# Optimization experiments

Hardware: AMD Instinct MI355X
Metric: run time of the kernel (lower is better)

## Reference

```python
import jax, jax.numpy as jnp
import numpy as np


def setup_inputs() -> dict:
    key = jax.random.key(0)
    k1, k2, k3 = jax.random.split(key, 3)
    B, S, E = 4, 4096, 512
    x = jax.random.normal(k1, (B, S, E), dtype=jnp.float32)
    # xavier_uniform for Linear weights; zero biases (per _reset_parameters)
    lim_qkv = float(np.sqrt(6.0 / (E + 3 * E)))
    W_qkv = jax.random.uniform(k2, (3 * E, E), minval=-lim_qkv, maxval=lim_qkv, dtype=jnp.float32)
    b_qkv = jnp.zeros((3 * E,), dtype=jnp.float32)
    lim_out = float(np.sqrt(6.0 / (E + E)))
    W_out = jax.random.uniform(k3, (E, E), minval=-lim_out, maxval=lim_out, dtype=jnp.float32)
    b_out = jnp.zeros((E,), dtype=jnp.float32)
    return {"x": x, "W_qkv": W_qkv, "b_qkv": b_qkv, "W_out": W_out, "b_out": b_out}


def reference(x, W_qkv, b_qkv, W_out, b_out):
    B, S, E = x.shape
    H = 8
    D = E // H
    qkv = x @ W_qkv.T + b_qkv                      # [B,S,3E]
    qkv = qkv.reshape(B, S, H, 3 * D)
    q, k, v = jnp.split(qkv, 3, axis=-1)            # each [B,S,H,D]
    q = jax.nn.sigmoid(q)
    k = jax.nn.sigmoid(k)
    # flow conservation normalizers (sum over seq dim=1, then feature dim=3)
    i = jnp.sum(q * jnp.sum(k, axis=1, keepdims=True), axis=3, keepdims=True)      # [B,S,H,1]
    o = jnp.sum(k * jnp.sum(q, axis=1, keepdims=True), axis=3, keepdims=True)
    i_hat = jnp.sum(q * jnp.sum(k / o, axis=1, keepdims=True), axis=3, keepdims=True)
    o_hat = jnp.sum(k * jnp.sum(q / i, axis=1, keepdims=True), axis=3, keepdims=True)
    # NOTE: faithful to source — matmul batches over (B,S) and contracts the HEAD axis
    vw = v * jax.nn.softmax(o_hat, axis=1)          # [B,S,H,D]
    kv = jnp.einsum('bshd,bshe->bsde', k, vw)       # [B,S,D,D]
    r = jnp.einsum('bshd,bsde->bshe', q / i, kv) * jax.nn.sigmoid(i_hat)  # [B,S,H,D]
    values = r.reshape(B, S, E)
    return values @ W_out.T + b_out
```

## Files before the change

### kernel.cpp

```cpp
#include <hip/hip_runtime.h>
#include <cstdint>
#include <cstddef>

#define B_ 4
#define S_ 4096
#define E_ 512
#define NPOS 16384
#define QKVC 1536
#define K_ 512

typedef unsigned short u16;
typedef u16    u16x8  __attribute__((ext_vector_type(8)));
typedef u16    u16x4  __attribute__((ext_vector_type(4)));
typedef __bf16 bf16x8 __attribute__((ext_vector_type(8)));
typedef float  f32x4  __attribute__((ext_vector_type(4)));

__device__ __forceinline__ u16 f2bf(float f) {
    unsigned u = __builtin_bit_cast(unsigned, f);
    unsigned r = (u + 0x7fffu + ((u >> 16) & 1u)) >> 16;
    return (u16)r;
}
__device__ __forceinline__ float bf2f(u16 u) {
    return __builtin_bit_cast(float, (unsigned)u << 16);
}
__device__ __forceinline__ float rcpf(float x) { return __builtin_amdgcn_rcpf(x); }

__device__ __forceinline__ void async16(const void* g, void* lds) {
    __builtin_amdgcn_global_load_lds(
        (const __attribute__((address_space(1))) unsigned int*)g,
        (__attribute__((address_space(3))) unsigned int*)lds, 16, 0, 0);
}

__global__ void cvt_kernel(const float4* __restrict__ in, u16x4* __restrict__ out, int n4) {
    int i = blockIdx.x * 256 + threadIdx.x;
    if (i < n4) {
        float4 v = in[i];
        u16x4 o;
        o[0] = f2bf(v.x); o[1] = f2bf(v.y); o[2] = f2bf(v.z); o[3] = f2bf(v.w);
        out[i] = o;
    }
}

__device__ __forceinline__ void mfma_step(const u16* AsB, const u16* BsB,
                                          int wm, int wn, int fr, int fkk,
                                          f32x4 (&acc)[4][4]) {
    bf16x8 a[4], b[4];
    #pragma unroll
    for (int i = 0; i < 4; ++i)
        a[i] = *(const bf16x8*)&AsB[(wm + i * 16 + fr) * 32 + fkk];
    #pragma unroll
    for (int j = 0; j < 4; ++j)
        b[j] = *(const bf16x8*)&BsB[(wn + j * 16 + fr) * 32 + fkk];
    __builtin_amdgcn_s_setprio(1);
    #pragma unroll
    for (int i = 0; i < 4; ++i)
        #pragma unroll
        for (int j = 0; j < 4; ++j)
            acc[i][j] = __builtin_amdgcn_mfma_f32_16x16x32_bf16(a[i], b[j], acc[i][j], 0, 0, 0);
    __builtin_amdgcn_s_setprio(0);
}

__global__ __launch_bounds__(256) void gemm_qkv(
        const u16* __restrict__ A, const u16* __restrict__ Bw,
        const float* __restrict__ bias,
        u16* __restrict__ Qb, u16* __restrict__ Kb, u16* __restrict__ Vb,
        int K) {
    __shared__ u16 As[2][128 * 32];
    __shared__ u16 Bs[2][128 * 32];
    const int tid  = threadIdx.x;
    const int wave = tid >> 6, lane = tid & 63;
    const int m0 = blockIdx.y * 128, n0 = blockIdx.x * 128;
    const int wm = (wave & 1) * 64, wn = (wave >> 1) * 64;

    const int srow = wave * 16 + (lane >> 2);
    const int cgs  = (lane & 3) ^ ((lane >> 2) & 3) ^ ((lane >> 4) & 3);
    const u16* Ap = A  + (size_t)(m0 + srow) * K + cgs * 8;
    const u16* Bp = Bw + (size_t)(n0 + srow) * K + cgs * 8;
    const int woff = wave * 512;
    const size_t rstep = (size_t)64 * K;

    f32x4 acc[4][4] = {};
    const int fr  = lane & 15;
    const int fkk = (((lane >> 4) ^ (fr & 3) ^ ((fr >> 2) & 3))) * 8;

    async16(Ap,         &As[0][woff]);
    async16(Ap + rstep, &As[0][woff + 2048]);
    async16(Bp,         &Bs[0][woff]);
    async16(Bp + rstep, &Bs[0][woff + 2048]);
    __syncthreads();

    int cur = 0;
    for (int k0 = 32; k0 < K; k0 += 32) {
        const int nxt = cur ^ 1;
        async16(Ap + k0,         &As[nxt][woff]);
        async16(Ap + k0 + rstep, &As[nxt][woff + 2048]);
        async16(Bp + k0,         &Bs[nxt][woff]);
        async16(Bp + k0 + rstep, &Bs[nxt][woff + 2048]);
        mfma_step(As[cur], Bs[cur], wm, wn, fr, fkk, acc);
        __syncthreads();
        cur = nxt;
    }
    mfma_step(As[cur], Bs[cur], wm, wn, fr, fkk, acc);

    const int cn = lane & 15, rb = (lane >> 4) * 4;
    const int cg   = (n0 + wn) >> 6;
    const int type = cg % 3;
    const int hb   = cg / 3;
    u16* dst = (type == 0) ? Qb : (type == 1) ? Kb : Vb;
    const bool sg = (type < 2);
    #pragma unroll
    for (int i = 0; i < 4; ++i) {
        int mbase = m0 + wm + i * 16 + rb;
        #pragma unroll
        for (int j = 0; j < 4; ++j) {
            int ccol = j * 16 + cn;
            float bv = bias[n0 + wn + ccol];
            int outcol = hb * 64 + ccol;
            f32x4 av = acc[i][j];
            #pragma unroll
            for (int r = 0; r < 4; ++r) {
                float v = av[r] + bv;
                if (sg) v = 1.f / (1.f + __expf(-v));
                dst[(size_t)(mbase + r) * 512 + outcol] = f2bf(v);
            }
        }
    }
}

__global__ __launch_bounds__(256) void gemm_out(
        const u16* __restrict__ A, const u16* __restrict__ Bw,
        const float* __restrict__ bias, float* __restrict__ C,
        int N, int K) {
    __shared__ u16 As[2][128 * 32];
    __shared__ u16 Bs[2][128 * 32];
    const int tid  = threadIdx.x;
    const int wave = tid >> 6, lane = tid & 63;
    const int m0 = blockIdx.y * 128, n0 = blockIdx.x * 128;
    const int wm = (wave & 1) * 64, wn = (wave >> 1) * 64;
    const int srow = wave * 16 + (lane >> 2);
    const int cgs  = (lane & 3) ^ ((lane >> 2) & 3) ^ ((lane >> 4) & 3);
    const u16* Ap = A  + (size_t)(m0 + srow) * K + cgs * 8;
    const u16* Bp = Bw + (size_t)(n0 + srow) * K + cgs * 8;
    const int woff = wave * 512;
    const size_t rstep = (size_t)64 * K;
    f32x4 acc[4][4] = {};
    const int fr  = lane & 15;
    const int fkk = (((lane >> 4) ^ (fr & 3) ^ ((fr >> 2) & 3))) * 8;

    async16(Ap,         &As[0][woff]);
    async16(Ap + rstep, &As[0][woff + 2048]);
    async16(Bp,         &Bs[0][woff]);
    async16(Bp + rstep, &Bs[0][woff + 2048]);
    __syncthreads();

    int cur = 0;
    for (int k0 = 32; k0 < K; k0 += 32) {
        const int nxt = cur ^ 1;
        async16(Ap + k0,         &As[nxt][woff]);
        async16(Ap + k0 + rstep, &As[nxt][woff + 2048]);
        async16(Bp + k0,         &Bs[nxt][woff]);
        async16(Bp + k0 + rstep, &Bs[nxt][woff + 2048]);
        mfma_step(As[cur], Bs[cur], wm, wn, fr, fkk, acc);
        __syncthreads();
        cur = nxt;
    }
    mfma_step(As[cur], Bs[cur], wm, wn, fr, fkk, acc);

    const int cn = lane & 15, rb = (lane >> 4) * 4;
    #pragma unroll
    for (int i = 0; i < 4; ++i) {
        int mbase = m0 + wm + i * 16 + rb;
        #pragma unroll
        for (int j = 0; j < 4; ++j) {
            int nn = n0 + wn + j * 16 + cn;
            float bv = bias[nn];
            f32x4 av = acc[i][j];
            #pragma unroll
            for (int r = 0; r < 4; ++r)
                C[(size_t)(mbase + r) * N + nn] = av[r] + bv;
        }
    }
}

__global__ __launch_bounds__(256) void sum_qk(const u16* __restrict__ Qg, const u16* __restrict__ Kg,
                                              float* __restrict__ sumq, float* __restrict__ sumk) {
    int b = blockIdx.x, sc = blockIdx.y;
    int w = threadIdx.x >> 6, lane = threadIdx.x & 63;
    float aq[8] = {}, ak[8] = {};
    int p0 = b * S_ + sc * 32 + w * 8;
    for (int it = 0; it < 8; ++it) {
        size_t off = (size_t)(p0 + it) * 512 + lane * 8;
        u16x8 q8 = *(const u16x8*)(Qg + off);
        u16x8 k8 = *(const u16x8*)(Kg + off);
        #pragma unroll
        for (int j = 0; j < 8; ++j) { aq[j] += bf2f(q8[j]); ak[j] += bf2f(k8[j]); }
    }
    __shared__ float red[4][1024];
    #pragma unroll
    for (int j = 0; j < 8; ++j) {
        red[w][lane * 8 + j]       = aq[j];
        red[w][512 + lane * 8 + j] = ak[j];
    }
    __syncthreads();
    int t = threadIdx.x;
    #pragma unroll
    for (int rr = 0; rr < 4; ++rr) {
        int slot = rr * 256 + t;
        float s = red[0][slot] + red[1][slot] + red[2][slot] + red[3][slot];
        float* dst = (slot < 512) ? &sumq[b * 512 + slot] : &sumk[b * 512 + (slot - 512)];
        atomicAdd(dst, s);
    }
}

__global__ __launch_bounds__(256) void fused_io(const u16* __restrict__ Qg, const u16* __restrict__ Kg,
                                                const float* __restrict__ sumq, const float* __restrict__ sumk,
                                                float* __restrict__ iv,
                                                float* __restrict__ sumqi, float* __restrict__ sumko) {
    int b = blockIdx.x, sc = blockIdx.y;
    int w = threadIdx.x >> 6, lane = threadIdx.x & 63;
    float skL[8], sqL[8];
    #pragma unroll
    for (int j = 0; j < 8; ++j) {
        skL[j] = sumk[b * 512 + lane * 8 + j];
        sqL[j] = sumq[b * 512 + lane * 8 + j];
    }
    float aqi[8] = {}, ako[8] = {};
    int p0 = b * S_ + sc * 32 + w * 8;
    for (int it = 0; it < 8; ++it) {
        int p = p0 + it;
        size_t off = (size_t)p * 512 + lane * 8;
        u16x8 q8 = *(const u16x8*)(Qg + off);
        u16x8 k8 = *(const u16x8*)(Kg + off);
        float qf[8], kf[8];
        #pragma unroll
        for (int j = 0; j < 8; ++j) { qf[j] = bf2f(q8[j]); kf[j] = bf2f(k8[j]); }
        float di = 0.f, dox = 0.f;
        #pragma unroll
        for (int j = 0; j < 8; ++j) { di += qf[j] * skL[j]; dox += kf[j] * sqL[j]; }
        di  += __shfl_xor(di, 1);  di  += __shfl_xor(di, 2);  di  += __shfl_xor(di, 4);
        dox += __shfl_xor(dox, 1); dox += __shfl_xor(dox, 2); dox += __shfl_xor(dox, 4);
        if ((lane & 7) == 0) iv[(size_t)p * 8 + (lane >> 3)] = di;
        float ri = rcpf(di), ro = rcpf(dox);
        #pragma unroll
        for (int j = 0; j < 8; ++j) { aqi[j] += qf[j] * ri; ako[j] += kf[j] * ro; }
    }
    __shared__ float red[4][1024];
    #pragma unroll
    for (int j = 0; j < 8; ++j) {
        red[w][lane * 8 + j]       = aqi[j];
        red[w][512 + lane * 8 + j] = ako[j];
    }
    __syncthreads();
    int t = threadIdx.x;
    #pragma unroll
    for (int rr = 0; rr < 4; ++rr) {
        int slot = rr * 256 + t;
        float s = red[0][slot] + red[1][slot] + red[2][slot] + red[3][slot];
        float* dst = (slot < 512) ? &sumqi[b * 512 + slot] : &sumko[b * 512 + (slot - 512)];
        atomicAdd(dst, s);
    }
}

__global__ __launch_bounds__(256) void io2_kernel(const u16* __restrict__ Qg, const u16* __restrict__ Kg,
                                                  const float* __restrict__ sumqi, const float* __restrict__ sumko,
                                                  const float* __restrict__ iv,
                                                  float* __restrict__ rowsc, float* __restrict__ wexp,
                                                  float* __restrict__ sm) {
    int b = blockIdx.x, sc = blockIdx.y;
    int w = threadIdx.x >> 6, lane = threadIdx.x & 63;
    float skoL[8], sqiL[8];
    #pragma unroll
    for (int j = 0; j < 8; ++j) {
        skoL[j] = sumko[b * 512 + lane * 8 + j];
        sqiL[j] = sumqi[b * 512 + lane * 8 + j];
    }
    float smacc = 0.f;
    int p0 = b * S_ + sc * 32 + w * 8;
    for (int it = 0; it < 8; ++it) {
        int p = p0 + it;
        size_t off = (size_t)p * 512 + lane * 8;
        u16x8 q8 = *(const u16x8*)(Qg + off);
        u16x8 k8 = *(const u16x8*)(Kg + off);
        float dih = 0.f, doh = 0.f;
        #pragma unroll
        for (int j = 0; j < 8; ++j) {
            dih += bf2f(q8[j]) * skoL[j];
            doh += bf2f(k8[j]) * sqiL[j];
        }
        dih += __shfl_xor(dih, 1); dih += __shfl_xor(dih, 2); dih += __shfl_xor(dih, 4);
        doh += __shfl_xor(doh, 1); doh += __shfl_xor(doh, 2); doh += __shfl_xor(doh, 4);
        if ((lane & 7) == 0) {
            int h = lane >> 3;
            float sig = 1.f / (1.f + __expf(-dih));
            rowsc[(size_t)p * 8 + h] = sig * rcpf(iv[(size_t)p * 8 + h]);
            float we = __expf(fminf(doh, 80.f));
            wexp[(size_t)p * 8 + h] = we;
            smacc += we;
        }
    }
    __shared__ float sr[4][8];
    if ((lane & 7) == 0) sr[w][lane >> 3] = smacc;
    __syncthreads();
    if (threadIdx.x < 8)
        atomicAdd(&sm[b * 8 + threadIdx.x],
                  sr[0][threadIdx.x] + sr[1][threadIdx.x] + sr[2][threadIdx.x] + sr[3][threadIdx.x]);
}

__global__ __launch_bounds__(256) void finalize_kernel(
        const u16* __restrict__ Qg, const u16* __restrict__ Kg, const u16* __restrict__ Vg,
        const float* __restrict__ rowsc, const float* __restrict__ wexp, const float* __restrict__ sm,
        u16* __restrict__ Rg) {
    __shared__ float Ml[4][2][8][9];
    __shared__ float vw[4][2][8][68];
    int w = threadIdx.x >> 6, lane = threadIdx.x & 63;
    int p0 = (blockIdx.x * 4 + w) * 2;
    int b = p0 >> 12;

    {
        int pl = (lane >> 3) & 1, hh = lane & 7, quad = lane >> 4;
        const u16* qa = Qg + (size_t)(p0 + pl) * 512 + hh * 64 + quad * 8;
        const u16* ka = Kg + (size_t)(p0 + pl) * 512 + hh * 64 + quad * 8;
        bf16x8 a0 = __builtin_bit_cast(bf16x8, *(const u16x8*)qa);
        bf16x8 a1 = __builtin_bit_cast(bf16x8, *(const u16x8*)(qa + 32));
        bf16x8 b0 = __builtin_bit_cast(bf16x8, *(const u16x8*)ka);
        bf16x8 b1 = __builtin_bit_cast(bf16x8, *(const u16x8*)(ka + 32));
        f32x4 accm = {0.f, 0.f, 0.f, 0.f};
        accm = __builtin_amdgcn_mfma_f32_16x16x32_bf16(a0, b0, accm, 0, 0, 0);
        accm = __builtin_amdgcn_mfma_f32_16x16x32_bf16(a1, b1, accm, 0, 0, 0);
        if (((lane >> 5) & 1) == ((lane >> 3) & 1)) {
            int plm = lane >> 5, hr = ((lane >> 4) & 1) * 4, h2 = lane & 7;
            #pragma unroll
            for (int r = 0; r < 4; ++r) Ml[w][plm][hr + r][h2] = accm[r];
        }
    }
    {
        int hv = lane >> 3, e0 = (lane & 7) * 8;
        float invsm = rcpf(sm[b * 8 + hv]);
        #pragma unroll
        for (int pl = 0; pl < 2; ++pl) {
            u16x8 v8 = *(const u16x8*)(Vg + (size_t)(p0 + pl) * 512 + lane * 8);
            float wgt = wexp[(size_t)(p0 + pl) * 8 + hv] * invsm;
            f32x4 x0, x1;
            #pragma unroll
            for (int j = 0; j < 4; ++j) { x0[j] = bf2f(v8[j]) * wgt; x1[j] = bf2f(v8[4 + j]) * wgt; }
            *(f32x4*)&vw[w][pl][hv][e0]     = x0;
            *(f32x4*)&vw[w][pl][hv][e0 + 4] = x1;
        }
    }
    __syncthreads();
    {
        int pl = lane >> 5, idx = lane & 31, h = idx >> 2, eq = (idx & 3) * 16;
        float out[16] = {};
        #pragma unroll
        for (int h2 = 0; h2 < 8; ++h2) {
            float m = Ml[w][pl][h][h2];
            #pragma unroll
            for (int c = 0; c < 4; ++c) {
                f32x4 vv = *(const f32x4*)&vw[w][pl][h2][eq + c * 4];
                #pragma unroll
                for (int j = 0; j < 4; ++j) out[c * 4 + j] += m * vv[j];
            }
        }
        float rs = rowsc[(size_t)(p0 + pl) * 8 + h];
        u16x8 o0, o1;
        #pragma unroll
        for (int j = 0; j < 8; ++j) { o0[j] = f2bf(out[j] * rs); o1[j] = f2bf(out[8 + j] * rs); }
        u16* dst = Rg + (size_t)(p0 + pl) * 512 + h * 64 + eq;
        *(u16x8*)dst       = o0;
        *(u16x8*)(dst + 8) = o1;
    }
}

extern "C" void kernel_launch(void* const* d_in, const int* in_sizes, int n_in,
                              void* d_out, int out_size, void* d_ws, size_t ws_size,
                              hipStream_t stream) {
    const float* x    = (const float*)d_in[0];
    const float* Wqkv = (const float*)d_in[1];
    const float* bqkv = (const float*)d_in[2];
    const float* Wout = (const float*)d_in[3];
    const float* bout = (const float*)d_in[4];
    float* out = (float*)d_out;
    char* ws = (char*)d_ws;

    constexpr size_t SZ_XBF  = (size_t)NPOS * E_ * 2;
    constexpr size_t SZ_WQBF = (size_t)QKVC * E_ * 2;
    constexpr size_t SZ_WOBF = (size_t)E_ * E_ * 2;
    constexpr size_t SZ_QKVB = (size_t)NPOS * E_ * 2;
    constexpr size_t SZ_SUM  = (size_t)B_ * 512 * 4;
    constexpr size_t SZ_V8   = (size_t)NPOS * 8 * 4;

    size_t off = 0;
    u16*   xbf   = (u16*)(ws + off);   off += SZ_XBF;
    u16*   wqbf  = (u16*)(ws + off);   off += SZ_WQBF;
    u16*   wobf  = (u16*)(ws + off);   off += SZ_WOBF;
    u16*   Qb    = (u16*)(ws + off);   off += SZ_QKVB;
    u16*   Kb    = (u16*)(ws + off);   off += SZ_QKVB;
    u16*   Vb    = (u16*)(ws + off);   off += SZ_QKVB;
    char*  zbase = ws + off;
    float* sumq  = (float*)(ws + off); off += SZ_SUM;
    float* sumk  = (float*)(ws + off); off += SZ_SUM;
    float* sumqi = (float*)(ws + off); off += SZ_SUM;
    float* sumko = (float*)(ws + off); off += SZ_SUM;
    float* sm    = (float*)(ws + off); off += 256;
    size_t zlen  = (char*)(ws + off) - zbase;
    float* iv    = (float*)(ws + off); off += SZ_V8;
    float* rowsc = (float*)(ws + off); off += SZ_V8;
    float* wexp  = (float*)(ws + off); off += SZ_V8;
    u16*   rbf   = xbf;

    hipMemsetAsync(zbase, 0, zlen, stream);

    cvt_kernel<<<(NPOS * E_ / 4) / 256, 256, 0, stream>>>((const float4*)x, (u16x4*)xbf, NPOS * E_ / 4);
    cvt_kernel<<<(QKVC * E_ / 4) / 256, 256, 0, stream>>>((const float4*)Wqkv, (u16x4*)wqbf, QKVC * E_ / 4);
    cvt_kernel<<<(E_ * E_ / 4) / 256, 256, 0, stream>>>((const float4*)Wout, (u16x4*)wobf, E_ * E_ / 4);

    gemm_qkv<<<dim3(QKVC / 128, NPOS / 128), 256, 0, stream>>>(xbf, wqbf, bqkv, Qb, Kb, Vb, K_);

    sum_qk<<<dim3(B_, 128), 256, 0, stream>>>(Qb, Kb, sumq, sumk);
    fused_io<<<dim3(B_, 128), 256, 0, stream>>>(Qb, Kb, sumq, sumk, iv, sumqi, sumko);
    io2_kernel<<<dim3(B_, 128), 256, 0, stream>>>(Qb, Kb, sumqi, sumko, iv, rowsc, wexp, sm);
    finalize_kernel<<<NPOS / 8, 256, 0, stream>>>(Qb, Kb, Vb, rowsc, wexp, sm, rbf);

    gemm_out<<<dim3(E_ / 128, NPOS / 128), 256, 0, stream>>>(rbf, wobf, bout, out, E_, K_);
}
```

Before: 200.8 us.

## Triple-buffer GEMM pipeline and fuse seq-sum of sigmoid Q/K into QKV epilogue

Replaces the double-buffered K loop in both GEMMs with a three-stage async-load pipeline that waits with partial vmcnt and a raw barrier, so global loads for tile t+2 overlap compute on tile t. It also accumulates per-column sums of the sigmoid Q and K values in the QKV GEMM epilogue and reduces them with atomics, which removes the separate sum_qk kernel and its re-read of Q and K. The cost is more LDS per block, which may lower occupancy, plus extra atomics. The sums are taken from fp32 values before bf16 rounding, so they differ slightly from the old sums.

```diff
diff --git a/kernel.cpp b/kernel.cpp
--- a/kernel.cpp
+++ b/kernel.cpp
@@ -60,13 +60,39 @@
     __builtin_amdgcn_s_setprio(0);
 }
 
+#define GEMM_PIPELINE(NT)                                                     \
+    {                                                                          \
+        STAGE(0, 0);                                                           \
+        STAGE(1, 1);                                                           \
+        asm volatile("s_waitcnt vmcnt(4)" ::: "memory");                       \
+        __builtin_amdgcn_s_barrier();                                          \
+        __builtin_amdgcn_sched_barrier(0);                                     \
+        int cb = 0, sb = 1;                                                    \
+        for (int t = 0; t < (NT) - 2; ++t) {                                   \
+            sb = (sb == 2) ? 0 : sb + 1;                                       \
+            STAGE(t + 2, sb);                                                  \
+            mfma_step(As[cb], Bs[cb], wm, wn, fr, fkk, acc);                   \
+            asm volatile("s_waitcnt vmcnt(4)" ::: "memory");                   \
+            __builtin_amdgcn_s_barrier();                                      \
+            __builtin_amdgcn_sched_barrier(0);                                 \
+            cb = (cb == 2) ? 0 : cb + 1;                                       \
+        }                                                                      \
+        mfma_step(As[cb], Bs[cb], wm, wn, fr, fkk, acc);                       \
+        asm volatile("s_waitcnt vmcnt(0)" ::: "memory");                       \
+        __builtin_amdgcn_s_barrier();                                          \
+        __builtin_amdgcn_sched_barrier(0);                                     \
+        cb = (cb == 2) ? 0 : cb + 1;                                           \
+        mfma_step(As[cb], Bs[cb], wm, wn, fr, fkk, acc);                       \
+    }
+
 __global__ __launch_bounds__(256) void gemm_qkv(
         const u16* __restrict__ A, const u16* __restrict__ Bw,
         const float* __restrict__ bias,
         u16* __restrict__ Qb, u16* __restrict__ Kb, u16* __restrict__ Vb,
+        float* __restrict__ sumq, float* __restrict__ sumk,
         int K) {
-    __shared__ u16 As[2][128 * 32];
-    __shared__ u16 Bs[2][128 * 32];
+    __shared__ u16 As[3][128 * 32];
+    __shared__ u16 Bs[3][128 * 32];
     const int tid  = threadIdx.x;
     const int wave = tid >> 6, lane = tid & 63;
     const int m0 = blockIdx.y * 128, n0 = blockIdx.x * 128;
@@ -83,24 +109,15 @@
     const int fr  = lane & 15;
     const int fkk = (((lane >> 4) ^ (fr & 3) ^ ((fr >> 2) & 3))) * 8;
 
-    async16(Ap,         &As[0][woff]);
-    async16(Ap + rstep, &As[0][woff + 2048]);
-    async16(Bp,         &Bs[0][woff]);
-    async16(Bp + rstep, &Bs[0][woff + 2048]);
-    __syncthreads();
-
-    int cur = 0;
-    for (int k0 = 32; k0 < K; k0 += 32) {
-        const int nxt = cur ^ 1;
-        async16(Ap + k0,         &As[nxt][woff]);
-        async16(Ap + k0 + rstep, &As[nxt][woff + 2048]);
-        async16(Bp + k0,         &Bs[nxt][woff]);
-        async16(Bp + k0 + rstep, &Bs[nxt][woff + 2048]);
-        mfma_step(As[cur], Bs[cur], wm, wn, fr, fkk, acc);
-        __syncthreads();
-        cur = nxt;
-    }
-    mfma_step(As[cur], Bs[cur], wm, wn, fr, fkk, acc);
+    #define STAGE(t, buf)                                             \
+        async16(Ap + (t) * 32,         &As[buf][woff]);               \
+        async16(Ap + (t) * 32 + rstep, &As[buf][woff + 2048]);        \
+        async16(Bp + (t) * 32,         &Bs[buf][woff]);               \
+        async16(Bp + (t) * 32 + rstep, &Bs[buf][woff + 2048]);
+
+    const int nt = K >> 5;
+    GEMM_PIPELINE(nt)
+    #undef STAGE
 
     const int cn = lane & 15, rb = (lane >> 4) * 4;
     const int cg   = (n0 + wn) >> 6;
@@ -108,6 +125,7 @@
     const int hb   = cg / 3;
     u16* dst = (type == 0) ? Qb : (type == 1) ? Kb : Vb;
     const bool sg = (type < 2);
+    float colsum[4] = {};
     #pragma unroll
     for (int i = 0; i < 4; ++i) {
         int mbase = m0 + wm + i * 16 + rb;
@@ -120,9 +138,21 @@
             #pragma unroll
             for (int r = 0; r < 4; ++r) {
                 float v = av[r] + bv;
-                if (sg) v = 1.f / (1.f + __expf(-v));
+                if (sg) { v = 1.f / (1.f + __expf(-v)); colsum[j] += v; }
                 dst[(size_t)(mbase + r) * 512 + outcol] = f2bf(v);
             }
+        }
+    }
+    if (sg) {
+        float* sdst = (type == 0) ? sumq : sumk;
+        const int b = m0 >> 12;
+        #pragma unroll
+        for (int j = 0; j < 4; ++j) {
+            float s = colsum[j];
+            s += __shfl_xor(s, 16);
+            s += __shfl_xor(s, 32);
+            if (lane < 16)
+                atomicAdd(&sdst[b * 512 + hb * 64 + j * 16 + cn], s);
         }
     }
 }
@@ -131,8 +161,8 @@
         const u16* __restrict__ A, const u16* __restrict__ Bw,
         const float* __restrict__ bias, float* __restrict__ C,
         int N, int K) {
-    __shared__ u16 As[2][128 * 32];
-    __shared__ u16 Bs[2][128 * 32];
+    __shared__ u16 As[3][128 * 32];
+    __shared__ u16 Bs[3][128 * 32];
     const int tid  = threadIdx.x;
     const int wave = tid >> 6, lane = tid & 63;
     const int m0 = blockIdx.y * 128, n0 = blockIdx.x * 128;
@@ -147,24 +177,15 @@
     const int fr  = lane & 15;
     const int fkk = (((lane >> 4) ^ (fr & 3) ^ ((fr >> 2) & 3))) * 8;
 
-    async16(Ap,         &As[0][woff]);
-    async16(Ap + rstep, &As[0][woff + 2048]);
-    async16(Bp,         &Bs[0][woff]);
-    async16(Bp + rstep, &Bs[0][woff + 2048]);
-    __syncthreads();
-
-    int cur = 0;
-    for (int k0 = 32; k0 < K; k0 += 32) {
-        const int nxt = cur ^ 1;
-        async16(Ap + k0,         &As[nxt][woff]);
-        async16(Ap + k0 + rstep, &As[nxt][woff + 2048]);
-        async16(Bp + k0,         &Bs[nxt][woff]);
-        async16(Bp + k0 + rstep, &Bs[nxt][woff + 2048]);
-        mfma_step(As[cur], Bs[cur], wm, wn, fr, fkk, acc);
-        __syncthreads();
-        cur = nxt;
-    }
-    mfma_step(As[cur], Bs[cur], wm, wn, fr, fkk, acc);
+    #define STAGE(t, buf)                                             \
+        async16(Ap + (t) * 32,         &As[buf][woff]);               \
+        async16(Ap + (t) * 32 + rstep, &As[buf][woff + 2048]);        \
+        async16(Bp + (t) * 32,         &Bs[buf][woff]);               \
+        async16(Bp + (t) * 32 + rstep, &Bs[buf][woff + 2048]);
+
+    const int nt = K >> 5;
+    GEMM_PIPELINE(nt)
+    #undef STAGE
 
     const int cn = lane & 15, rb = (lane >> 4) * 4;
     #pragma unroll
@@ -179,36 +200,6 @@
             for (int r = 0; r < 4; ++r)
                 C[(size_t)(mbase + r) * N + nn] = av[r] + bv;
         }
-    }
-}
-
-__global__ __launch_bounds__(256) void sum_qk(const u16* __restrict__ Qg, const u16* __restrict__ Kg,
-                                              float* __restrict__ sumq, float* __restrict__ sumk) {
-    int b = blockIdx.x, sc = blockIdx.y;
-    int w = threadIdx.x >> 6, lane = threadIdx.x & 63;
-    float aq[8] = {}, ak[8] = {};
-    int p0 = b * S_ + sc * 32 + w * 8;
-    for (int it = 0; it < 8; ++it) {
-        size_t off = (size_t)(p0 + it) * 512 + lane * 8;
-        u16x8 q8 = *(const u16x8*)(Qg + off);
-        u16x8 k8 = *(const u16x8*)(Kg + off);
-        #pragma unroll
-        for (int j = 0; j < 8; ++j) { aq[j] += bf2f(q8[j]); ak[j] += bf2f(k8[j]); }
-    }
-    __shared__ float red[4][1024];
-    #pragma unroll
-    for (int j = 0; j < 8; ++j) {
-        red[w][lane * 8 + j]       = aq[j];
-        red[w][512 + lane * 8 + j] = ak[j];
-    }
-    __syncthreads();
-    int t = threadIdx.x;
-    #pragma unroll
-    for (int rr = 0; rr < 4; ++rr) {
-        int slot = rr * 256 + t;
-        float s = red[0][slot] + red[1][slot] + red[2][slot] + red[3][slot];
-        float* dst = (slot < 512) ? &sumq[b * 512 + slot] : &sumk[b * 512 + (slot - 512)];
-        atomicAdd(dst, s);
     }
 }
 
@@ -414,9 +405,8 @@
     cvt_kernel<<<(QKVC * E_ / 4) / 256, 256, 0, stream>>>((const float4*)Wqkv, (u16x4*)wqbf, QKVC * E_ / 4);
     cvt_kernel<<<(E_ * E_ / 4) / 256, 256, 0, stream>>>((const float4*)Wout, (u16x4*)wobf, E_ * E_ / 4);
 
-    gemm_qkv<<<dim3(QKVC / 128, NPOS / 128), 256, 0, stream>>>(xbf, wqbf, bqkv, Qb, Kb, Vb, K_);
-
-    sum_qk<<<dim3(B_, 128), 256, 0, stream>>>(Qb, Kb, sumq, sumk);
+    gemm_qkv<<<dim3(QKVC / 128, NPOS / 128), 256, 0, stream>>>(xbf, wqbf, bqkv, Qb, Kb, Vb, sumq, sumk, K_);
+
     fused_io<<<dim3(B_, 128), 256, 0, stream>>>(Qb, Kb, sumq, sumk, iv, sumqi, sumko);
     io2_kernel<<<dim3(B_, 128), 256, 0, stream>>>(Qb, Kb, sumqi, sumko, iv, rowsc, wexp, sm);
     finalize_kernel<<<NPOS / 8, 256, 0, stream>>>(Qb, Kb, Vb, rowsc, wexp, sm, rbf);
```

Result: faster. 192.0 us (-4.4%).
